# Performance work log

Hardware: AMD Instinct MI355X
Metric: run time of the kernel (lower is better)

## Reference

```python
import jax, jax.numpy as jnp
import numpy as np

N = 100000
C_IN = 256
C_OUT = 256
LN_EPS = 1e-5


def setup_inputs() -> dict:
    key = jax.random.key(0)
    ks = jax.random.split(key, 6)
    x = jax.random.normal(ks[0], (N, C_IN), dtype=jnp.float32)
    idx1 = jax.random.randint(ks[1], (N,), 0, N, dtype=jnp.int64 if jax.config.jax_enable_x64 else jnp.int32)
    idx2 = jax.random.randint(ks[2], (N,), 0, N, dtype=idx1.dtype)
    idx3 = jax.random.randint(ks[3], (N,), 0, N, dtype=idx1.dtype)
    idx4 = jax.random.randint(ks[4], (N,), 0, N, dtype=idx1.dtype)
    W = jax.random.normal(ks[5], (5 * C_IN, C_OUT), dtype=jnp.float32) * (1.0 / np.sqrt(5 * C_IN))
    b = jnp.zeros((C_OUT,), dtype=jnp.float32)
    gamma = jnp.ones((C_OUT,), dtype=jnp.float32)
    beta = jnp.zeros((C_OUT,), dtype=jnp.float32)
    return {"x": x, "idx1": idx1, "idx2": idx2, "idx3": idx3, "idx4": idx4,
            "W": W, "b": b, "gamma": gamma, "beta": beta}


def reference(x, idx1, idx2, idx3, idx4, W, b, gamma, beta):
    # Four sparse-mm neighbor gathers (one nonzero of value 1 per row)
    a = x[idx1]
    bb = x[idx2]
    c = x[idx3]
    d = x[idx4]
    # symmetric combine + concat -> [N, 5*C_IN]
    patch = jnp.concatenate([x, jnp.abs(a - c), a + c, jnp.abs(bb - d), bb + d], axis=-1)
    y = patch @ W + b
    # LayerNorm over channels
    mu = jnp.mean(y, axis=-1, keepdims=True)
    var = jnp.mean(jnp.square(y - mu), axis=-1, keepdims=True)
    y = (y - mu) * jax.lax.rsqrt(var + LN_EPS) * gamma + beta
    # residual (in_channels == out_channels -> identity projection)
    y = y + x
    # torch nn.GELU default is exact (erf) gelu
    return jax.nn.gelu(y, approximate=False)
```

## Files before the change

### kernel.cpp

```cpp
#include <hip/hip_runtime.h>


#define N_ROWS   100000
#define C        256
#define BK       32
#define NCHUNK   40
#define BM       64
#define CHUNK_EL (C * BK)
#define LN_EPS   1e-5f

typedef __bf16 bf16;
typedef bf16  bf16x8 __attribute__((ext_vector_type(8)));
typedef float f32x4  __attribute__((ext_vector_type(4)));

union BV  { bf16x8 v; bf16 h[8]; };
union FV2 { float4 q[2]; float f[8]; };

__device__ __forceinline__ void async_g2l(const void* g, void* l) {
    __builtin_amdgcn_global_load_lds(
        (const __attribute__((address_space(1))) void*)g,
        (__attribute__((address_space(3))) void*)l, 16, 0, 0);
}

__global__ void wprep(const float* __restrict__ W, bf16* __restrict__ Wt) {
    int t = blockIdx.x * 256 + threadIdx.x;
    if (t >= NCHUNK * BK * C) return;
    int n  = t & 255;
    int r  = t >> 8;
    int kc = r >> 5;
    int kk = r & 31;
    int kRow;
    if (kc < 8)       kRow = kc * 32 + kk;
    else if (kc < 24) { int u = kc - 8;  kRow = 256 + (u & 1) * 256 + (u >> 1) * 32 + kk; }
    else              { int u = kc - 24; kRow = 768 + (u & 1) * 256 + (u >> 1) * 32 + kk; }
    int gs = (kk >> 3) ^ ((n >> 1) & 3);
    Wt[(size_t)kc * CHUNK_EL + n * 32 + gs * 8 + (kk & 7)] = (bf16)W[(size_t)kRow * C + n];
}

__global__ __launch_bounds__(256, 3)
void fused(const float* __restrict__ x,
           const int* __restrict__ idx1, const int* __restrict__ idx2,
           const int* __restrict__ idx3, const int* __restrict__ idx4,
           const bf16* __restrict__ Wt,
           const float* __restrict__ bias,
           const float* __restrict__ gamma_, const float* __restrict__ beta_,
           float* __restrict__ out)
{
    __shared__ __align__(16) bf16 Wl[2][CHUNK_EL];
    __shared__ __align__(16) union {
        bf16 a[2][BM * BK];
        struct { float rsum[BM][4]; float rsq[BM][4]; float mu[BM]; float rs[BM]; } red;
    } SA;

    const int tid  = threadIdx.x;
    const int lane = tid & 63;
    const int wv   = tid >> 6;
    const int quad = lane >> 4;
    const int l16  = lane & 15;
    const int r0   = blockIdx.x * BM;

    const int r_st = tid >> 2;
    const int q_st = tid & 3;
    int gr_self = r0 + r_st; if (gr_self >= N_ROWS) gr_self = 0;
    const int ia = idx1[gr_self], ib = idx2[gr_self];
    const int ic = idx3[gr_self], id = idx4[gr_self];

    const int aswz = ((q_st ^ ((r_st >> 1) & 3)) << 3);
    const int a_w_off = r_st * 32 + aswz;

    f32x4 acc[4][4] = {};
    bf16x8 hold;

    {
        const float4* p = (const float4*)(x + (size_t)gr_self * C + (q_st << 3));
        FV2 u; u.q[0] = p[0]; u.q[1] = p[1];
        BV b0;
        #pragma unroll
        for (int j = 0; j < 8; ++j) b0.h[j] = (bf16)u.f[j];
        *(bf16x8*)&SA.a[0][a_w_off] = b0.v;
        #pragma unroll
        for (int j = 0; j < 4; ++j) {
            int g = j * 256 + tid;
            async_g2l(Wt + g * 8, &Wl[0][g * 8]);
        }
    }
    __syncthreads();

    for (int kc = 0; kc < NCHUNK; ++kc) {
        const int kn = kc + 1;

        if (kn < NCHUNK) {
            const bf16* wsrc = Wt + (size_t)kn * CHUNK_EL;
            bf16* wdst = Wl[kn & 1];
            #pragma unroll
            for (int j = 0; j < 4; ++j) {
                int g = j * 256 + tid;
                async_g2l(wsrc + g * 8, wdst + g * 8);
            }
        }

        FV2 la, lc;
        int mode = 0;
        if (kn < 8) {
            mode = 1;
            const float4* p = (const float4*)(x + (size_t)gr_self * C + (kn << 5) + (q_st << 3));
            la.q[0] = p[0]; la.q[1] = p[1];
        } else if (kn < NCHUNK) {
            int u = (kn < 24) ? (kn - 8) : (kn - 24);
            if (!(u & 1)) {
                mode = 2;
                int rA = (kn < 24) ? ia : ib;
                int rC = (kn < 24) ? ic : id;
                int off = ((u >> 1) << 5) + (q_st << 3);
                const float4* pa = (const float4*)(x + (size_t)rA * C + off);
                const float4* pc = (const float4*)(x + (size_t)rC * C + off);
                la.q[0] = pa[0]; la.q[1] = pa[1];
                lc.q[0] = pc[0]; lc.q[1] = pc[1];
            }
        }

        {
            const bf16* Ab = SA.a[kc & 1];
            const bf16* Wb = Wl[kc & 1];
            bf16x8 af[4], wf[4];
            #pragma unroll
            for (int mi = 0; mi < 4; ++mi) {
                int m = mi * 16 + l16;
                af[mi] = *(const bf16x8*)&Ab[m * 32 + ((quad ^ ((m >> 1) & 3)) << 3)];
            }
            #pragma unroll
            for (int ni = 0; ni < 4; ++ni) {
                int n = wv * 64 + ni * 16 + l16;
                wf[ni] = *(const bf16x8*)&Wb[n * 32 + ((quad ^ ((n >> 1) & 3)) << 3)];
            }
            #pragma unroll
            for (int mi = 0; mi < 4; ++mi)
                #pragma unroll
                for (int ni = 0; ni < 4; ++ni)
                    acc[mi][ni] = __builtin_amdgcn_mfma_f32_16x16x32_bf16(
                        af[mi], wf[ni], acc[mi][ni], 0, 0, 0);
        }

        if (kn < NCHUNK) {
            BV sv;
            if (mode == 1) {
                #pragma unroll
                for (int j = 0; j < 8; ++j) sv.h[j] = (bf16)la.f[j];
            } else if (mode == 2) {
                BV hs;
                #pragma unroll
                for (int j = 0; j < 8; ++j) {
                    sv.h[j] = (bf16)fabsf(la.f[j] - lc.f[j]);
                    hs.h[j] = (bf16)(la.f[j] + lc.f[j]);
                }
                hold = hs.v;
            } else {
                sv.v = hold;
            }
            *(bf16x8*)&SA.a[kn & 1][a_w_off] = sv.v;
            __syncthreads();
        }
    }

    float bcol[4], gcol[4], ecol[4];
    #pragma unroll
    for (int ni = 0; ni < 4; ++ni) {
        int cidx = wv * 64 + ni * 16 + l16;
        bcol[ni] = bias[cidx]; gcol[ni] = gamma_[cidx]; ecol[ni] = beta_[cidx];
    }
    #pragma unroll
    for (int mi = 0; mi < 4; ++mi)
        #pragma unroll
        for (int ni = 0; ni < 4; ++ni)
            #pragma unroll
            for (int rg = 0; rg < 4; ++rg)
                acc[mi][ni][rg] += bcol[ni];

    #pragma unroll
    for (int mi = 0; mi < 4; ++mi) {
        #pragma unroll
        for (int rg = 0; rg < 4; ++rg) {
            float s = 0.f, q = 0.f;
            #pragma unroll
            for (int ni = 0; ni < 4; ++ni) {
                float y = acc[mi][ni][rg];
                s += y; q += y * y;
            }
            #pragma unroll
            for (int m = 1; m <= 8; m <<= 1) {
                s += __shfl_xor(s, m, 64);
                q += __shfl_xor(q, m, 64);
            }
            if (l16 == 0) {
                int row = mi * 16 + quad * 4 + rg;
                SA.red.rsum[row][wv] = s;
                SA.red.rsq [row][wv] = q;
            }
        }
    }
    __syncthreads();
    if (tid < BM) {
        float s  = SA.red.rsum[tid][0] + SA.red.rsum[tid][1] + SA.red.rsum[tid][2] + SA.red.rsum[tid][3];
        float q  = SA.red.rsq [tid][0] + SA.red.rsq [tid][1] + SA.red.rsq [tid][2] + SA.red.rsq [tid][3];
        float mu = s * (1.0f / C);
        float var = q * (1.0f / C) - mu * mu;
        SA.red.mu[tid] = mu;
        SA.red.rs[tid] = rsqrtf(var + LN_EPS);
    }
    __syncthreads();

    #pragma unroll
    for (int mi = 0; mi < 4; ++mi) {
        #pragma unroll
        for (int rg = 0; rg < 4; ++rg) {
            int row  = mi * 16 + quad * 4 + rg;
            int grow = r0 + row;
            if (grow >= N_ROWS) continue;
            float mu = SA.red.mu[row], rs = SA.red.rs[row];
            #pragma unroll
            for (int ni = 0; ni < 4; ++ni) {
                int cidx = wv * 64 + ni * 16 + l16;
                float y = (acc[mi][ni][rg] - mu) * rs * gcol[ni] + ecol[ni];
                y += x[(size_t)grow * C + cidx];
                float g = 0.5f * y * (1.0f + erff(y * 0.70710678118654752f));
                out[(size_t)grow * C + cidx] = g;
            }
        }
    }
}

extern "C" void kernel_launch(void* const* d_in, const int* in_sizes, int n_in,
                              void* d_out, int out_size, void* d_ws, size_t ws_size,
                              hipStream_t stream) {
    const float* x  = (const float*)d_in[0];
    const int*   i1 = (const int*)d_in[1];
    const int*   i2 = (const int*)d_in[2];
    const int*   i3 = (const int*)d_in[3];
    const int*   i4 = (const int*)d_in[4];
    const float* W  = (const float*)d_in[5];
    const float* b  = (const float*)d_in[6];
    const float* gm = (const float*)d_in[7];
    const float* bt = (const float*)d_in[8];
    float* outp = (float*)d_out;
    bf16* Wt = (bf16*)d_ws;

    wprep<<<(NCHUNK * BK * C + 255) / 256, 256, 0, stream>>>(W, Wt);
    fused<<<(N_ROWS + BM - 1) / BM, 256, 0, stream>>>(
        x, i1, i2, i3, i4, Wt, b, gm, bt, outp);
}
```

Before: 364.0 us.

## Load weight fragments directly into registers instead of staging through LDS

The weight matrix is pre-packed into the exact per-lane MFMA fragment order, so each wave loads its B-operand fragments straight from global memory (L2-resident) into registers, prefetching the next chunk. This removes the LDS weight buffers, the async global-to-LDS copies and the LDS reads for W, which shrinks shared memory use. The barrier becomes a lighter lgkmcnt wait plus s_barrier, and MFMA issue priority is raised with setprio. The cost is more global load traffic per wave, since each of the 4 waves fetches its own slice for every block with no sharing, plus extra registers for the prefetch buffers.

```diff
diff --git a/kernel.cpp b/kernel.cpp
--- a/kernel.cpp
+++ b/kernel.cpp
@@ -6,7 +6,7 @@
 #define BK       32
 #define NCHUNK   40
 #define BM       64
-#define CHUNK_EL (C * BK)
+#define CHUNK_V  1024
 #define LN_EPS   1e-5f
 
 typedef __bf16 bf16;
@@ -16,25 +16,28 @@
 union BV  { bf16x8 v; bf16 h[8]; };
 union FV2 { float4 q[2]; float f[8]; };
 
-__device__ __forceinline__ void async_g2l(const void* g, void* l) {
-    __builtin_amdgcn_global_load_lds(
-        (const __attribute__((address_space(1))) void*)g,
-        (__attribute__((address_space(3))) void*)l, 16, 0, 0);
-}
+#define LBAR() asm volatile("s_waitcnt lgkmcnt(0)\n\ts_barrier" ::: "memory")
 
 __global__ void wprep(const float* __restrict__ W, bf16* __restrict__ Wt) {
     int t = blockIdx.x * 256 + threadIdx.x;
-    if (t >= NCHUNK * BK * C) return;
-    int n  = t & 255;
-    int r  = t >> 8;
-    int kc = r >> 5;
-    int kk = r & 31;
-    int kRow;
-    if (kc < 8)       kRow = kc * 32 + kk;
-    else if (kc < 24) { int u = kc - 8;  kRow = 256 + (u & 1) * 256 + (u >> 1) * 32 + kk; }
-    else              { int u = kc - 24; kRow = 768 + (u & 1) * 256 + (u >> 1) * 32 + kk; }
-    int gs = (kk >> 3) ^ ((n >> 1) & 3);
-    Wt[(size_t)kc * CHUNK_EL + n * 32 + gs * 8 + (kk & 7)] = (bf16)W[(size_t)kRow * C + n];
+    if (t >= NCHUNK * 4 * 4 * 64) return;
+    int lane = t & 63;
+    int ni   = (t >> 6) & 3;
+    int wv   = (t >> 8) & 3;
+    int kc   = t >> 10;
+    int l16  = lane & 15, quad = lane >> 4;
+    int n = wv * 64 + ni * 16 + l16;
+    int base;
+    if (kc < 8)       base = kc * 32;
+    else if (kc < 24) { int u = kc - 8;  base = 256 + (u & 1) * 256 + (u >> 1) * 32; }
+    else              { int u = kc - 24; base = 768 + (u & 1) * 256 + (u >> 1) * 32; }
+    BV o;
+    #pragma unroll
+    for (int e = 0; e < 8; ++e) {
+        int kRow = base + quad * 8 + e;
+        o.h[e] = (bf16)W[(size_t)kRow * C + n];
+    }
+    ((bf16x8*)Wt)[t] = o.v;
 }
 
 __global__ __launch_bounds__(256, 3)
@@ -46,7 +49,6 @@
            const float* __restrict__ gamma_, const float* __restrict__ beta_,
            float* __restrict__ out)
 {
-    __shared__ __align__(16) bf16 Wl[2][CHUNK_EL];
     __shared__ __align__(16) union {
         bf16 a[2][BM * BK];
         struct { float rsum[BM][4]; float rsq[BM][4]; float mu[BM]; float rs[BM]; } red;
@@ -65,39 +67,34 @@
     const int ia = idx1[gr_self], ib = idx2[gr_self];
     const int ic = idx3[gr_self], id = idx4[gr_self];
 
-    const int aswz = ((q_st ^ ((r_st >> 1) & 3)) << 3);
-    const int a_w_off = r_st * 32 + aswz;
+    const int a_w_off = r_st * 32 + ((q_st ^ ((r_st >> 1) & 3)) << 3);
+    int a_r_off[4];
+    #pragma unroll
+    for (int mi = 0; mi < 4; ++mi) {
+        int m = mi * 16 + l16;
+        a_r_off[mi] = m * 32 + ((quad ^ ((m >> 1) & 3)) << 3);
+    }
+
+    const bf16x8* Wq = (const bf16x8*)Wt + wv * 256 + lane;
 
     f32x4 acc[4][4] = {};
     bf16x8 hold;
+    bf16x8 wf[4], wfn[4];
 
     {
         const float4* p = (const float4*)(x + (size_t)gr_self * C + (q_st << 3));
         FV2 u; u.q[0] = p[0]; u.q[1] = p[1];
+        #pragma unroll
+        for (int j = 0; j < 4; ++j) wf[j] = Wq[j * 64];
         BV b0;
         #pragma unroll
         for (int j = 0; j < 8; ++j) b0.h[j] = (bf16)u.f[j];
         *(bf16x8*)&SA.a[0][a_w_off] = b0.v;
-        #pragma unroll
-        for (int j = 0; j < 4; ++j) {
-            int g = j * 256 + tid;
-            async_g2l(Wt + g * 8, &Wl[0][g * 8]);
-        }
-    }
-    __syncthreads();
+    }
+    LBAR();
 
     for (int kc = 0; kc < NCHUNK; ++kc) {
         const int kn = kc + 1;
-
-        if (kn < NCHUNK) {
-            const bf16* wsrc = Wt + (size_t)kn * CHUNK_EL;
-            bf16* wdst = Wl[kn & 1];
-            #pragma unroll
-            for (int j = 0; j < 4; ++j) {
-                int g = j * 256 + tid;
-                async_g2l(wsrc + g * 8, wdst + g * 8);
-            }
-        }
 
         FV2 la, lc;
         int mode = 0;
@@ -119,26 +116,26 @@
             }
         }
 
+        if (kn < NCHUNK) {
+            const bf16x8* wp = Wq + (size_t)kn * CHUNK_V;
+            #pragma unroll
+            for (int j = 0; j < 4; ++j) wfn[j] = wp[j * 64];
+        }
+
         {
             const bf16* Ab = SA.a[kc & 1];
-            const bf16* Wb = Wl[kc & 1];
-            bf16x8 af[4], wf[4];
-            #pragma unroll
-            for (int mi = 0; mi < 4; ++mi) {
-                int m = mi * 16 + l16;
-                af[mi] = *(const bf16x8*)&Ab[m * 32 + ((quad ^ ((m >> 1) & 3)) << 3)];
-            }
-            #pragma unroll
-            for (int ni = 0; ni < 4; ++ni) {
-                int n = wv * 64 + ni * 16 + l16;
-                wf[ni] = *(const bf16x8*)&Wb[n * 32 + ((quad ^ ((n >> 1) & 3)) << 3)];
-            }
+            bf16x8 af[4];
+            #pragma unroll
+            for (int mi = 0; mi < 4; ++mi)
+                af[mi] = *(const bf16x8*)&Ab[a_r_off[mi]];
+            __builtin_amdgcn_s_setprio(1);
             #pragma unroll
             for (int mi = 0; mi < 4; ++mi)
                 #pragma unroll
                 for (int ni = 0; ni < 4; ++ni)
                     acc[mi][ni] = __builtin_amdgcn_mfma_f32_16x16x32_bf16(
                         af[mi], wf[ni], acc[mi][ni], 0, 0, 0);
+            __builtin_amdgcn_s_setprio(0);
         }
 
         if (kn < NCHUNK) {
@@ -158,7 +155,9 @@
                 sv.v = hold;
             }
             *(bf16x8*)&SA.a[kn & 1][a_w_off] = sv.v;
-            __syncthreads();
+            #pragma unroll
+            for (int j = 0; j < 4; ++j) wf[j] = wfn[j];
+            LBAR();
         }
     }
 
@@ -244,7 +243,7 @@
     float* outp = (float*)d_out;
     bf16* Wt = (bf16*)d_ws;
 
-    wprep<<<(NCHUNK * BK * C + 255) / 256, 256, 0, stream>>>(W, Wt);
+    wprep<<<(NCHUNK * 4 * 4 * 64 + 255) / 256, 256, 0, stream>>>(W, Wt);
     fused<<<(N_ROWS + BM - 1) / BM, 256, 0, stream>>>(
         x, i1, i2, i3, i4, Wt, b, gm, bt, outp);
 }
```

After: 346.3 us. 4.9% less time.
